# Performance work log

Measured on AMD Instinct MI355X. Metric: run time of the kernel, lower is better.

The kernel has to match this reference:

```python
import jax, jax.numpy as jnp
import numpy as np

D, VH, DFF, NL, VOCAB, NH, NKV, HD, R, SCALE = 4096, 1024, 14336, 2, 32000, 32, 8, 128, 8, 4.0
B, NIMG, T = 2, 257, 511
S = NIMG + T

def _rmsnorm(x, w, eps=1e-5):
    v = jnp.mean(jnp.square(x), axis=-1, keepdims=True)
    return x * jax.lax.rsqrt(v + eps) * w

def _lora(x, W, A, Bm):
    # base (dequantized NF4 equivalent) matmul + low-rank LoRA path, scaling = alpha/r
    base = jnp.einsum('...d,od->...o', x, W)
    low = jnp.einsum('...r,or->...o', jnp.einsum('...d,rd->...r', x, A), Bm)
    return base + low * SCALE

def _rope_tables(s):
    inv = 1.0 / (10000.0 ** (jnp.arange(0, HD, 2, dtype=jnp.float32) / HD))
    ang = jnp.arange(s, dtype=jnp.float32)[:, None] * inv[None, :]
    c, sn = jnp.cos(ang), jnp.sin(ang)
    return jnp.concatenate([c, c], -1), jnp.concatenate([sn, sn], -1)

def _apply_rope(x, cos, sin):
    rot = jnp.concatenate([-x[..., HD // 2:], x[..., :HD // 2]], -1)
    return x * cos + rot * sin

def _forward(image_embeds, proj_W, proj_b, embed, ln1, ln2, ln_f, Wq, Aq, Bq, Wk, Ak, Bk, Wv, Av, Bv, Wo, Ao, Bo, Wg, Ag, Bg, Wu, Au, Bu, Wd, Ad, Bd, input_ids, attention_mask):
    b = image_embeds.shape[0]
    img = jnp.einsum('bsv,dv->bsd', image_embeds, proj_W) + proj_b  # projector
    txt = embed[input_ids]                                          # token embedding lookup
    h = jnp.concatenate([img, txt], axis=1)                         # (B, S, D)
    s = h.shape[1]
    cos, sin = _rope_tables(s)
    allow = jnp.tril(jnp.ones((s, s), bool))[None, None] & (attention_mask[:, None, None, :] > 0)
    for i in range(NL):
        x = _rmsnorm(h, ln1[i])
        q = _lora(x, Wq[i], Aq[i], Bq[i]).reshape(b, s, NH, HD).transpose(0, 2, 1, 3)
        k = _lora(x, Wk[i], Ak[i], Bk[i]).reshape(b, s, NKV, HD).transpose(0, 2, 1, 3)
        v = _lora(x, Wv[i], Av[i], Bv[i]).reshape(b, s, NKV, HD).transpose(0, 2, 1, 3)
        q = _apply_rope(q, cos, sin)
        k = _apply_rope(k, cos, sin)
        k = jnp.repeat(k, NH // NKV, axis=1)  # GQA: expand kv heads
        v = jnp.repeat(v, NH // NKV, axis=1)
        scores = jnp.einsum('bhsd,bhtd->bhst', q, k) / jnp.sqrt(jnp.float32(HD))
        scores = jnp.where(allow, scores, jnp.float32(-1e30))
        attn = jnp.einsum('bhst,bhtd->bhsd', jax.nn.softmax(scores, axis=-1), v)
        attn = attn.transpose(0, 2, 1, 3).reshape(b, s, D)
        h = h + _lora(attn, Wo[i], Ao[i], Bo[i])
        x = _rmsnorm(h, ln2[i])
        h = h + _lora(jax.nn.silu(_lora(x, Wg[i], Ag[i], Bg[i])) * _lora(x, Wu[i], Au[i], Bu[i]), Wd[i], Ad[i], Bd[i])
    return _rmsnorm(h, ln_f)  # HF hidden_states[-1] is post final norm

def setup_inputs():
    key = jax.random.key(0)
    ks = iter(jax.random.split(key, 40))
    n = lambda shape, sc=0.02: jax.random.normal(next(ks), shape, jnp.float32) * sc
    return dict(
        image_embeds=jax.random.normal(next(ks), (B, NIMG, VH), jnp.float32),
        input_ids=jax.random.randint(next(ks), (B, T), 0, VOCAB),
        attention_mask=jnp.ones((B, S), jnp.int32),
        proj_W=n((D, VH)), proj_b=jnp.zeros((D,), jnp.float32),
        embed=n((VOCAB, D)),
        ln1=jnp.ones((NL, D), jnp.float32), ln2=jnp.ones((NL, D), jnp.float32), ln_f=jnp.ones((D,), jnp.float32),
        Wq=n((NL, D, D)), Aq=n((NL, R, D)), Bq=n((NL, D, R)),
        Wk=n((NL, NKV * HD, D)), Ak=n((NL, R, D)), Bk=n((NL, NKV * HD, R)),
        Wv=n((NL, NKV * HD, D)), Av=n((NL, R, D)), Bv=n((NL, NKV * HD, R)),
        Wo=n((NL, D, D)), Ao=n((NL, R, D)), Bo=n((NL, D, R)),
        Wg=n((NL, DFF, D)), Ag=n((NL, R, D)), Bg=n((NL, DFF, R)),
        Wu=n((NL, DFF, D)), Au=n((NL, R, D)), Bu=n((NL, DFF, R)),
        Wd=n((NL, D, DFF)), Ad=n((NL, R, DFF)), Bd=n((NL, D, R)),
    )

def reference(image_embeds, input_ids, attention_mask, proj_W, proj_b, embed, ln1, ln2, ln_f, Wq, Aq, Bq, Wk, Ak, Bk, Wv, Av, Bv, Wo, Ao, Bo, Wg, Ag, Bg, Wu, Au, Bu, Wd, Ad, Bd):
    return _forward(image_embeds, proj_W, proj_b, embed, ln1, ln2, ln_f, Wq, Aq, Bq, Wk, Ak, Bk, Wv, Av, Bv, Wo, Ao, Bo, Wg, Ag, Bg, Wu, Au, Bu, Wd, Ad, Bd, input_ids, attention_mask)
```

## Files before the change

kernel.cpp:

```cpp
#include <hip/hip_runtime.h>
#include <hip/hip_bf16.h>
#include <cstdint>
#include <cstddef>

typedef unsigned short u16;
typedef unsigned int u32;
typedef __attribute__((ext_vector_type(8))) short short8;
typedef __attribute__((ext_vector_type(4))) short short4v;
typedef __attribute__((ext_vector_type(4))) float f32x4;

__device__ __forceinline__ u16 f2bf(float f) {
  u32 u = __float_as_uint(f);
  u32 r = (u + 0x7FFFu + ((u >> 16) & 1u)) >> 16;
  return (u16)r;
}
__device__ __forceinline__ float bf2f(u16 u) {
  return __uint_as_float(((u32)u) << 16);
}
__device__ __forceinline__ short f2bf_hw(float f) {
  union { __hip_bfloat16 h; u16 u; } c;
  c.h = __float2bfloat16(f);
  return (short)c.u;
}

__device__ __forceinline__ void gload_lds16(const void* g, void* l) {
  __builtin_amdgcn_global_load_lds((const __attribute__((address_space(1))) void*)g,
                                   (__attribute__((address_space(3))) void*)l, 16, 0, 0);
}

__global__ __launch_bounds__(256) void convert_w_kernel(const float* __restrict__ src,
    u16* __restrict__ dst, long n8) {
  long stride = (long)gridDim.x * 256;
  for (long i = (long)blockIdx.x * 256 + threadIdx.x; i < n8; i += stride) {
    const float* p = src + i * 8;
    float4 v0 = *(const float4*)p;
    float4 v1 = *(const float4*)(p + 4);
    uint4 w;
    w.x = (u32)(u16)f2bf_hw(v0.x) | ((u32)(u16)f2bf_hw(v0.y) << 16);
    w.y = (u32)(u16)f2bf_hw(v0.z) | ((u32)(u16)f2bf_hw(v0.w) << 16);
    w.z = (u32)(u16)f2bf_hw(v1.x) | ((u32)(u16)f2bf_hw(v1.y) << 16);
    w.w = (u32)(u16)f2bf_hw(v1.z) | ((u32)(u16)f2bf_hw(v1.w) << 16);
    *(uint4*)(dst + i * 8) = w;
  }
}

struct ConvJob { const float* src; u16* dst; long n8; };
struct GemmArgs {
  const u16* A; int M; int K; int lda;
  const float* W0; const float* LB0; int toff0;
  const float* W1; const float* LB1; int toff1;
  const float* W2; const float* LB2; int toff2;
  const u16* Wb0; const u16* Wb1; const u16* Wb2;
  int ldw;
  int seg1; int seg2;
  const float* t;
  const float* bias;
  const float* resid;
  float* outf; int ostride;
  u16* outb0; u16* outb1;
  int rowremap;
  float* outp;
  int ny_main;
  ConvJob cj[3];
};

template<int WMODE>
__global__ __launch_bounds__(256) void gemm_kernel(GemmArgs a) {
  __shared__ u16 Asm[2][128 * 64];
  __shared__ u16 BsmW[2][WMODE ? 128 * 64 : 128 * 128];
  const int tid = threadIdx.x;

  const int nconv = (int)gridDim.y - a.ny_main;
  if ((int)blockIdx.y < nconv) {
    if (blockIdx.z != 0) return;
    const long cb = (long)blockIdx.y * gridDim.x + blockIdx.x;
    const long cstr = (long)nconv * gridDim.x * 256;
#pragma unroll
    for (int j = 0; j < 3; j++) {
      const float* src = a.cj[j].src;
      if (!src) break;
      u16* dst = a.cj[j].dst;
      const long n8 = a.cj[j].n8;
      for (long i = cb * 256 + tid; i < n8; i += cstr) {
        const float* p = src + i * 8;
        float4 v0 = *(const float4*)p;
        float4 v1 = *(const float4*)(p + 4);
        uint4 w;
        w.x = (u32)(u16)f2bf_hw(v0.x) | ((u32)(u16)f2bf_hw(v0.y) << 16);
        w.y = (u32)(u16)f2bf_hw(v0.z) | ((u32)(u16)f2bf_hw(v0.w) << 16);
        w.z = (u32)(u16)f2bf_hw(v1.x) | ((u32)(u16)f2bf_hw(v1.y) << 16);
        w.w = (u32)(u16)f2bf_hw(v1.z) | ((u32)(u16)f2bf_hw(v1.w) << 16);
        *(uint4*)(dst + i * 8) = w;
      }
    }
    return;
  }
  const int yid = (int)blockIdx.y - nconv;

  const int nwg = gridDim.x * a.ny_main;
  const int bid0 = yid * gridDim.x + blockIdx.x;
  const int q = nwg >> 3, r = nwg & 7;
  const int xcd = bid0 & 7, pos = bid0 >> 3;
  const int nb = (xcd < r ? xcd * (q + 1) : r * (q + 1) + (xcd - r) * q) + pos;
  const int m0 = (nb % gridDim.x) * 128;
  const int n0 = (nb / gridDim.x) * 128;

  const float* W = a.W0; const u16* Wb = a.Wb0;
  const float* LB = a.LB0; int toff = a.toff0; int nbase = 0;
  if (a.seg2 && n0 >= a.seg2)      { W = a.W2; Wb = a.Wb2; LB = a.LB2; toff = a.toff2; nbase = a.seg2; }
  else if (a.seg1 && n0 >= a.seg1) { W = a.W1; Wb = a.Wb1; LB = a.LB1; toff = a.toff1; nbase = a.seg1; }
  const int koff = blockIdx.z * a.K;
  const u16* Ab = a.A + koff;
  const float* Wt = W + (size_t)(n0 - nbase) * a.ldw + koff;
  const u16* Wbt = Wb + (size_t)(n0 - nbase) * a.ldw + koff;

  const int lane = tid & 63, wid = tid >> 6;
  const int wr = wid >> 1, wcn = wid & 1;
  const int lrow = lane & 15, g = lane >> 4;
  const int arow = lane >> 3;
  const int aslot = (lane & 7) ^ arow;
  const int brow4 = lane >> 4;

  f32x4 acc[4][4] = {};

  auto dma_A = [&](int k0, int buf) {
#pragma unroll
    for (int i = 0; i < 4; i++) {
      int c = wid * 4 + i;
      const u16* src = Ab + (size_t)(m0 + c * 8 + arow) * a.lda + k0 + (aslot << 3);
      gload_lds16(src, &Asm[buf][c * 512]);
    }
  };
  auto dma_B = [&](int k0, int buf) {
    if (WMODE) {
#pragma unroll
      for (int i = 0; i < 4; i++) {
        int c = wid * 4 + i;
        const u16* src = Wbt + (size_t)(c * 8 + arow) * a.ldw + k0 + (aslot << 3);
        gload_lds16(src, &BsmW[buf][c * 512]);
      }
    } else {
      float* Bf = (float*)&BsmW[buf][0];
#pragma unroll
      for (int j = 0; j < 8; j++) {
        int rrow = wid * 32 + j * 4 + brow4;
        int sslot = (lane & 15) ^ (rrow & 7);
        const float* src = Wt + (size_t)rrow * a.ldw + k0 + (sslot << 2);
        gload_lds16(src, &Bf[(wid * 32 + j * 4) * 64]);
      }
    }
  };

  const int nk = a.K >> 6;
  dma_A(0, 0); dma_B(0, 0);
  if (nk > 1) { dma_A(64, 1); dma_B(64, 1); }

  for (int kt = 0; kt < nk; kt++) {
    const int cur = kt & 1;
    if (kt + 1 < nk) {
      if (WMODE) asm volatile("s_waitcnt vmcnt(8)" ::: "memory");
      else       asm volatile("s_waitcnt vmcnt(12)" ::: "memory");
    } else {
      asm volatile("s_waitcnt vmcnt(0)" ::: "memory");
    }
    __builtin_amdgcn_sched_barrier(0);
    __builtin_amdgcn_s_barrier();
    __builtin_amdgcn_sched_barrier(0);

    short8 af[4][2], bq[4][2];
#pragma unroll
    for (int mi = 0; mi < 4; mi++) {
      int row = wr * 64 + mi * 16 + lrow;
#pragma unroll
      for (int x = 0; x < 2; x++) {
        int s = x * 4 + g;
        af[mi][x] = *(const short8*)&Asm[cur][row * 64 + ((s ^ (lrow & 7)) << 3)];
      }
    }
#pragma unroll
    for (int ni = 0; ni < 4; ni++) {
      int row = wcn * 64 + ni * 16 + lrow;
      if (WMODE) {
#pragma unroll
        for (int x = 0; x < 2; x++) {
          int s = x * 4 + g;
          bq[ni][x] = *(const short8*)&BsmW[cur][row * 64 + ((s ^ (lrow & 7)) << 3)];
        }
      } else {
        const float* bp = (const float*)&BsmW[cur][0] + row * 64;
        int m = row & 7;
#pragma unroll
        for (int x = 0; x < 2; x++) {
          int sg0 = x * 8 + g * 2;
          f32x4 lo = *(const f32x4*)(bp + ((sg0 ^ m) << 2));
          f32x4 hi = *(const f32x4*)(bp + (((sg0 + 1) ^ m) << 2));
          short8 sv;
          sv[0] = f2bf_hw(lo[0]); sv[1] = f2bf_hw(lo[1]);
          sv[2] = f2bf_hw(lo[2]); sv[3] = f2bf_hw(lo[3]);
          sv[4] = f2bf_hw(hi[0]); sv[5] = f2bf_hw(hi[1]);
          sv[6] = f2bf_hw(hi[2]); sv[7] = f2bf_hw(hi[3]);
          bq[ni][x] = sv;
        }
      }
    }

    asm volatile("s_waitcnt lgkmcnt(0)" ::: "memory");
    __builtin_amdgcn_sched_barrier(0);
    __builtin_amdgcn_s_barrier();
    __builtin_amdgcn_sched_barrier(0);
    if (kt + 2 < nk) {
      dma_A((kt + 2) << 6, cur);
      dma_B((kt + 2) << 6, cur);
    }
    __builtin_amdgcn_sched_barrier(0);
#pragma unroll
    for (int x = 0; x < 2; x++)
#pragma unroll
      for (int mi = 0; mi < 4; mi++)
#pragma unroll
        for (int ni = 0; ni < 4; ni++)
          acc[mi][ni] = __builtin_amdgcn_mfma_f32_16x16x32_bf16(af[mi][x], bq[ni][x], acc[mi][ni], 0, 0, 0);
  }

  if (a.outp) {
    float* op = a.outp + (size_t)blockIdx.z * (1536 * 4096);
#pragma unroll
    for (int mi = 0; mi < 4; mi++)
#pragma unroll
      for (int rr = 0; rr < 4; rr++) {
        int row = m0 + wr * 64 + mi * 16 + (g << 2) + rr;
#pragma unroll
        for (int ni = 0; ni < 4; ni++) {
          int n = n0 + wcn * 64 + ni * 16 + lrow;
          op[(size_t)row * a.ostride + n] = acc[mi][ni][rr];
        }
      }
    return;
  }
  const bool dolora = (a.t != nullptr);
  float lbv[4][8];
#pragma unroll
  for (int ni = 0; ni < 4; ni++) {
    if (dolora) {
      int cl = wcn * 64 + ni * 16 + lrow;
      const float* bp = LB + (size_t)(n0 - nbase + cl) * 8;
#pragma unroll
      for (int r2 = 0; r2 < 8; r2++) lbv[ni][r2] = bp[r2];
    }
  }
#pragma unroll
  for (int mi = 0; mi < 4; mi++) {
#pragma unroll
    for (int rr = 0; rr < 4; rr++) {
      int row = m0 + wr * 64 + mi * 16 + (g << 2) + rr;
      if (row >= a.M) continue;
      float tv[8];
      if (dolora) {
        const float* tp = a.t + row * 32 + toff;
#pragma unroll
        for (int r2 = 0; r2 < 8; r2++) tv[r2] = tp[r2];
      }
#pragma unroll
      for (int ni = 0; ni < 4; ni++) {
        int n = n0 + wcn * 64 + ni * 16 + lrow;
        float val = acc[mi][ni][rr];
        if (dolora) {
          float ds = 0.f;
#pragma unroll
          for (int r2 = 0; r2 < 8; r2++) ds += tv[r2] * lbv[ni][r2];
          val += 4.0f * ds;
        }
        if (a.bias)  val += a.bias[n];
        if (a.resid) val += a.resid[(size_t)row * 4096 + n];
        if (a.outf) {
          int orow = a.rowremap ? (row < 257 ? row : row + 511) : row;
          a.outf[(size_t)orow * a.ostride + n] = val;
        } else if (a.seg1 && n >= a.seg1) {
          a.outb1[(size_t)row * a.ostride + (n - a.seg1)] = f2bf(val);
        } else {
          a.outb0[(size_t)row * a.ostride + n] = f2bf(val);
        }
      }
    }
  }
}

__global__ __launch_bounds__(256) void combine_kernel(float* __restrict__ h,
    const float* __restrict__ p, const float* __restrict__ t,
    const float* __restrict__ LB) {
  const int row = blockIdx.x;
  float tv[8];
  const float* tp = t + row * 32;
#pragma unroll
  for (int r = 0; r < 8; r++) tv[r] = tp[r];
  const float* p1 = p + (size_t)1536 * 4096;
#pragma unroll
  for (int i = 0; i < 4; i++) {
    int base = threadIdx.x * 4 + i * 1024;
    size_t off = (size_t)row * 4096 + base;
    float4 hv = *(const float4*)(h + off);
    float4 a0 = *(const float4*)(p + off);
    float4 a1 = *(const float4*)(p1 + off);
    float o[4] = {hv.x + a0.x + a1.x, hv.y + a0.y + a1.y,
                  hv.z + a0.z + a1.z, hv.w + a0.w + a1.w};
#pragma unroll
    for (int j = 0; j < 4; j++) {
      const float* lb = LB + (size_t)(base + j) * 8;
      float ds = 0.f;
#pragma unroll
      for (int r = 0; r < 8; r++) ds += tv[r] * lb[r];
      o[j] += 4.0f * ds;
    }
    float4 ov; ov.x = o[0]; ov.y = o[1]; ov.z = o[2]; ov.w = o[3];
    *(float4*)(h + off) = ov;
  }
}

template<int NA>
__global__ __launch_bounds__(256) void lora_xa_kernel(const u16* __restrict__ X, int K,
    const float* A0, const float* A1, const float* A2, float* __restrict__ t) {
  const int m = blockIdx.x;
  const u16* xr = X + (size_t)m * K;
  float acc[NA * 8];
#pragma unroll
  for (int i = 0; i < NA * 8; i++) acc[i] = 0.f;
  const float* Ap[3] = {A0, A1, A2};
  for (int k = threadIdx.x * 8; k < K; k += 2048) {
    uint4 xv = *(const uint4*)(xr + k);
    float xf[8];
    xf[0] = bf2f((u16)(xv.x & 0xffff)); xf[1] = bf2f((u16)(xv.x >> 16));
    xf[2] = bf2f((u16)(xv.y & 0xffff)); xf[3] = bf2f((u16)(xv.y >> 16));
    xf[4] = bf2f((u16)(xv.z & 0xffff)); xf[5] = bf2f((u16)(xv.z >> 16));
    xf[6] = bf2f((u16)(xv.w & 0xffff)); xf[7] = bf2f((u16)(xv.w >> 16));
#pragma unroll
    for (int aa = 0; aa < NA; aa++) {
#pragma unroll
      for (int r = 0; r < 8; r++) {
        const float* ar = Ap[aa] + (size_t)r * K + k;
        float4 a0 = *(const float4*)ar;
        float4 a1 = *(const float4*)(ar + 4);
        acc[aa * 8 + r] += xf[0] * a0.x + xf[1] * a0.y + xf[2] * a0.z + xf[3] * a0.w
                         + xf[4] * a1.x + xf[5] * a1.y + xf[6] * a1.z + xf[7] * a1.w;
      }
    }
  }
  __shared__ float red[4][NA * 8];
#pragma unroll
  for (int i = 0; i < NA * 8; i++) {
    float v = acc[i];
#pragma unroll
    for (int o = 1; o < 64; o <<= 1) v += __shfl_xor(v, o);
    if ((threadIdx.x & 63) == 0) red[threadIdx.x >> 6][i] = v;
  }
  __syncthreads();
  if (threadIdx.x < NA * 8)
    t[m * 32 + threadIdx.x] = red[0][threadIdx.x] + red[1][threadIdx.x]
                            + red[2][threadIdx.x] + red[3][threadIdx.x];
}

__global__ __launch_bounds__(256) void rmsnorm_kernel(const float* __restrict__ h,
    const float* __restrict__ w, u16* outb, float* outf) {
  const int m = blockIdx.x;
  const float* row = h + (size_t)m * 4096;
  float4 v[4];
  float ss = 0.f;
#pragma unroll
  for (int i = 0; i < 4; i++) {
    v[i] = *(const float4*)(row + threadIdx.x * 4 + i * 1024);
    ss += v[i].x * v[i].x + v[i].y * v[i].y + v[i].z * v[i].z + v[i].w * v[i].w;
  }
#pragma unroll
  for (int o = 1; o < 64; o <<= 1) ss += __shfl_xor(ss, o);
  __shared__ float red[4];
  if ((threadIdx.x & 63) == 0) red[threadIdx.x >> 6] = ss;
  __syncthreads();
  ss = red[0] + red[1] + red[2] + red[3];
  float rs = rsqrtf(ss * (1.f / 4096.f) + 1e-5f);
#pragma unroll
  for (int i = 0; i < 4; i++) {
    int base = threadIdx.x * 4 + i * 1024;
    float4 wv = *(const float4*)(w + base);
    float o0 = v[i].x * rs * wv.x, o1 = v[i].y * rs * wv.y;
    float o2 = v[i].z * rs * wv.z, o3 = v[i].w * rs * wv.w;
    if (outb) {
      short4v sv; sv.x = (short)f2bf(o0); sv.y = (short)f2bf(o1);
      sv.z = (short)f2bf(o2); sv.w = (short)f2bf(o3);
      *(short4v*)(outb + (size_t)m * 4096 + base) = sv;
    } else {
      float4 ov; ov.x = o0; ov.y = o1; ov.z = o2; ov.w = o3;
      *(float4*)(outf + (size_t)m * 4096 + base) = ov;
    }
  }
}

__global__ void rope_tab_kernel(float2* __restrict__ tab) {
  int idx = blockIdx.x * 256 + threadIdx.x;
  int s = idx >> 6, i = idx & 63;
  float inv = __expf(-(float)i * (9.210340371976184f / 64.f));
  float ang = (float)s * inv;
  float sn, cs;
  sincosf(ang, &sn, &cs);
  float2 r; r.x = cs; r.y = sn;
  tab[idx] = r;
}

__global__ __launch_bounds__(256) void rope_apply_kernel(float* __restrict__ qkv,
    const float2* __restrict__ tab) {
  int m = blockIdx.x;
  int s = m % 768;
  float* rowp = qkv + (size_t)m * 6144;
  for (int idx = threadIdx.x; idx < 2560; idx += 256) {
    int head = idx >> 6, i = idx & 63;
    int col = (head < 32) ? head * 128 : 4096 + (head - 32) * 128;
    float2 cs = tab[s * 64 + i];
    float x0 = rowp[col + i], x1 = rowp[col + i + 64];
    rowp[col + i]      = x0 * cs.x - x1 * cs.y;
    rowp[col + i + 64] = x1 * cs.x + x0 * cs.y;
  }
}

__global__ __launch_bounds__(256) void attn_mfma_kernel(const float* __restrict__ qkv,
    const int* __restrict__ amask, u16* __restrict__ attn_bf) {
  __shared__ u16 Ks[4][32][40];
  __shared__ u16 Vt[128][40];
  __shared__ u16 Ps[4][16][40];
  const int b = blockIdx.z, hh = blockIdx.y, q0 = blockIdx.x * 64;
  const int kvh = hh >> 2;
  const int tid = threadIdx.x, lane = tid & 63, w = tid >> 6;
  const int lrow = lane & 15, g = lane >> 4;
  const float sc = 0.08838834764831845f;

  short8 qf[4];
  {
    const float* qp = qkv + ((size_t)(b * 768 + q0 + w * 16 + lrow)) * 6144 + hh * 128;
#pragma unroll
    for (int ks = 0; ks < 4; ks++) {
      float4 lo = *(const float4*)(qp + ks * 32 + g * 8);
      float4 hi = *(const float4*)(qp + ks * 32 + g * 8 + 4);
      short8 sv;
      sv[0] = f2bf_hw(lo.x * sc); sv[1] = f2bf_hw(lo.y * sc);
      sv[2] = f2bf_hw(lo.z * sc); sv[3] = f2bf_hw(lo.w * sc);
      sv[4] = f2bf_hw(hi.x * sc); sv[5] = f2bf_hw(hi.y * sc);
      sv[6] = f2bf_hw(hi.z * sc); sv[7] = f2bf_hw(hi.w * sc);
      qf[ks] = sv;
    }
  }

  f32x4 acco[8] = {};
  float mrun[4] = {-1e30f, -1e30f, -1e30f, -1e30f};
  float lrun[4] = {0.f, 0.f, 0.f, 0.f};
  const int ntile = (q0 >> 5) + 2;

  for (int kt = 0; kt < ntile; kt++) {
    const int k0 = kt * 32;
    __syncthreads();
#pragma unroll
    for (int i = 0; i < 4; i++) {
      int idx = i * 256 + tid;
      int r2 = idx >> 5, c4 = (idx & 31) << 2;
      const float* kp = qkv + ((size_t)(b * 768 + k0 + r2)) * 6144 + 4096 + kvh * 128 + c4;
      float4 kv = *(const float4*)kp;
      short4v ksv;
      ksv.x = f2bf_hw(kv.x); ksv.y = f2bf_hw(kv.y);
      ksv.z = f2bf_hw(kv.z); ksv.w = f2bf_hw(kv.w);
      *(short4v*)&Ks[c4 >> 5][r2][c4 & 31] = ksv;
      float4 vv = *(const float4*)(kp + 1024);
      Vt[c4 + 0][r2] = (u16)f2bf_hw(vv.x);
      Vt[c4 + 1][r2] = (u16)f2bf_hw(vv.y);
      Vt[c4 + 2][r2] = (u16)f2bf_hw(vv.z);
      Vt[c4 + 3][r2] = (u16)f2bf_hw(vv.w);
    }
    __syncthreads();

    f32x4 s0 = {}, s1 = {};
#pragma unroll
    for (int ks = 0; ks < 4; ks++) {
      short8 kb0 = *(const short8*)&Ks[ks][lrow][g * 8];
      short8 kb1 = *(const short8*)&Ks[ks][16 + lrow][g * 8];
      s0 = __builtin_amdgcn_mfma_f32_16x16x32_bf16(qf[ks], kb0, s0, 0, 0, 0);
      s1 = __builtin_amdgcn_mfma_f32_16x16x32_bf16(qf[ks], kb1, s1, 0, 0, 0);
    }
    const int key0 = k0 + lrow, key1 = k0 + 16 + lrow;
    const bool am0 = amask[b * 768 + key0] != 0;
    const bool am1 = amask[b * 768 + key1] != 0;
    float scl4[4];
#pragma unroll
    for (int rr = 0; rr < 4; rr++) {
      int qrow = q0 + w * 16 + g * 4 + rr;
      float v0 = (key0 <= qrow && am0) ? s0[rr] : -1e30f;
      float v1 = (key1 <= qrow && am1) ? s1[rr] : -1e30f;
      float m = fmaxf(v0, v1);
      m = fmaxf(m, __shfl_xor(m, 1));
      m = fmaxf(m, __shfl_xor(m, 2));
      m = fmaxf(m, __shfl_xor(m, 4));
      m = fmaxf(m, __shfl_xor(m, 8));
      float mnew = fmaxf(mrun[rr], m);
      float scl = __expf(mrun[rr] - mnew);
      float p0 = __expf(v0 - mnew);
      float p1 = __expf(v1 - mnew);
      float ls = p0 + p1;
      ls += __shfl_xor(ls, 1);
      ls += __shfl_xor(ls, 2);
      ls += __shfl_xor(ls, 4);
      ls += __shfl_xor(ls, 8);
      lrun[rr] = lrun[rr] * scl + ls;
      mrun[rr] = mnew;
      scl4[rr] = scl;
      Ps[w][g * 4 + rr][lrow]      = (u16)f2bf_hw(p0);
      Ps[w][g * 4 + rr][16 + lrow] = (u16)f2bf_hw(p1);
    }
#pragma unroll
    for (int nf = 0; nf < 8; nf++)
#pragma unroll
      for (int rr = 0; rr < 4; rr++) acco[nf][rr] *= scl4[rr];

    asm volatile("s_waitcnt lgkmcnt(0)" ::: "memory");
    __builtin_amdgcn_sched_barrier(0);
    short8 pa = *(const short8*)&Ps[w][lrow][g * 8];
#pragma unroll
    for (int nf = 0; nf < 8; nf++) {
      short8 vb = *(const short8*)&Vt[nf * 16 + lrow][g * 8];
      acco[nf] = __builtin_amdgcn_mfma_f32_16x16x32_bf16(pa, vb, acco[nf], 0, 0, 0);
    }
  }

#pragma unroll
  for (int rr = 0; rr < 4; rr++) {
    float inv = 1.f / lrun[rr];
    size_t orow = (size_t)(b * 768 + q0 + w * 16 + g * 4 + rr);
#pragma unroll
    for (int nf = 0; nf < 8; nf++)
      attn_bf[orow * 4096 + hh * 128 + nf * 16 + lrow] = f2bf(acco[nf][rr] * inv);
  }
}

__global__ void convert_img_kernel(const float* __restrict__ in, u16* __restrict__ out) {
  int idx = blockIdx.x * 256 + threadIdx.x;
  if (idx >= 81920) return;
  uint4 w = {0u, 0u, 0u, 0u};
  if (idx < 65792) {
    const float* p = in + (size_t)idx * 8;
    float4 v0 = *(const float4*)p;
    float4 v1 = *(const float4*)(p + 4);
    w.x = (u32)f2bf(v0.x) | ((u32)f2bf(v0.y) << 16);
    w.y = (u32)f2bf(v0.z) | ((u32)f2bf(v0.w) << 16);
    w.z = (u32)f2bf(v1.x) | ((u32)f2bf(v1.y) << 16);
    w.w = (u32)f2bf(v1.z) | ((u32)f2bf(v1.w) << 16);
  }
  *(uint4*)(out + (size_t)idx * 8) = w;
}

__global__ void embed_gather_kernel(const float* __restrict__ embed,
    const int* __restrict__ ids, float* __restrict__ h) {
  int row = blockIdx.x;
  int b = row / 511, tt = row % 511;
  int id = ids[b * 511 + tt];
  const float* src = embed + (size_t)id * 4096;
  float* dst = h + ((size_t)(b * 768 + 257 + tt)) * 4096;
  for (int i = threadIdx.x * 4; i < 4096; i += 1024)
    *(float4*)(dst + i) = *(const float4*)(src + i);
}

__global__ __launch_bounds__(256) void gu_combine_kernel(const u16* __restrict__ g,
    const u16* __restrict__ u, u16* __restrict__ x2) {
  size_t idx = (size_t)blockIdx.x * 256 + threadIdx.x;
  uint4 gv = *(const uint4*)(g + idx * 8);
  uint4 uv = *(const uint4*)(u + idx * 8);
  u32 gi[4] = {gv.x, gv.y, gv.z, gv.w};
  u32 ui[4] = {uv.x, uv.y, uv.z, uv.w};
  u32 oi[4];
#pragma unroll
  for (int i = 0; i < 4; i++) {
    float g0 = bf2f((u16)(gi[i] & 0xffff)), g1 = bf2f((u16)(gi[i] >> 16));
    float u0 = bf2f((u16)(ui[i] & 0xffff)), u1 = bf2f((u16)(ui[i] >> 16));
    float s0 = g0 / (1.f + __expf(-g0)) * u0;
    float s1 = g1 / (1.f + __expf(-g1)) * u1;
    oi[i] = (u32)f2bf(s0) | ((u32)f2bf(s1) << 16);
  }
  uint4 ov; ov.x = oi[0]; ov.y = oi[1]; ov.z = oi[2]; ov.w = oi[3];
  *(uint4*)(x2 + idx * 8) = ov;
}

extern "C" void kernel_launch(void* const* d_in, const int* in_sizes, int n_in,
                              void* d_out, int out_size, void* d_ws, size_t ws_size,
                              hipStream_t stream) {
  const float* image_embeds = (const float*)d_in[0];
  const int*   input_ids    = (const int*)d_in[1];
  const int*   amask        = (const int*)d_in[2];
  const float* proj_W = (const float*)d_in[3];
  const float* proj_b = (const float*)d_in[4];
  const float* embed  = (const float*)d_in[5];
  const float* ln1 = (const float*)d_in[6];
  const float* ln2 = (const float*)d_in[7];
  const float* ln_f = (const float*)d_in[8];
  const float* Wq = (const float*)d_in[9];
  const float* Aq = (const float*)d_in[10];
  const float* Bq = (const float*)d_in[11];
  const float* Wk = (const float*)d_in[12];
  const float* Ak = (const float*)d_in[13];
  const float* Bk = (const float*)d_in[14];
  const float* Wv = (const float*)d_in[15];
  const float* Av = (const float*)d_in[16];
  const float* Bv = (const float*)d_in[17];
  const float* Wo = (const float*)d_in[18];
  const float* Ao = (const float*)d_in[19];
  const float* Bo = (const float*)d_in[20];
  const float* Wg = (const float*)d_in[21];
  const float* Ag = (const float*)d_in[22];
  const float* Bg = (const float*)d_in[23];
  const float* Wu = (const float*)d_in[24];
  const float* Au = (const float*)d_in[25];
  const float* Bu = (const float*)d_in[26];
  const float* Wd = (const float*)d_in[27];
  const float* Ad = (const float*)d_in[28];
  const float* Bd = (const float*)d_in[29];
  (void)in_sizes; (void)n_in; (void)out_size;

  char* ws = (char*)d_ws;
  size_t off = 0;
  auto alloc = [&](size_t bytes) -> void* {
    void* p = ws + off; off += (bytes + 255) & ~(size_t)255; return p;
  };
  float* h       = (float*) alloc((size_t)1536 * 4096 * 4);
  u16*   xn      = (u16*)   alloc((size_t)1536 * 4096 * 2);
  float* qkv     = (float*) alloc((size_t)1536 * 6144 * 4);
  u16*   attn_bf = (u16*)   alloc((size_t)1536 * 4096 * 2);
  u16*   g_bf    = (u16*)   alloc((size_t)1536 * 14336 * 2);
  u16*   u_bf    = (u16*)   alloc((size_t)1536 * 14336 * 2);
  u16*   x2_bf   = (u16*)   alloc((size_t)1536 * 14336 * 2);
  float* t       = (float*) alloc((size_t)1536 * 32 * 4);
  float2* tab    = (float2*)alloc((size_t)768 * 64 * 8);
  u16*   img_bf  = (u16*)   alloc((size_t)640 * 1024 * 2);
  float* pc      = (float*) alloc((size_t)2 * 1536 * 4096 * 4);
  const size_t nQ = (size_t)2 * 4096 * 4096;
  const size_t nK = (size_t)2 * 1024 * 4096;
  const size_t nG = (size_t)2 * 14336 * 4096;
  const long nQl8 = 4096L * 4096 / 8, nKl8 = 1024L * 4096 / 8, nGl8 = 14336L * 4096 / 8;
  u16* wq_b = (u16*)alloc(nQ * 2);
  u16* wk_b = (u16*)alloc(nK * 2);
  u16* wv_b = (u16*)alloc(nK * 2);
  u16* wo_b = (u16*)alloc(nQ * 2);
  u16* wg_b = (u16*)alloc(nG * 2);
  u16* wu_b = (u16*)alloc(nG * 2);
  u16* wd_b = (u16*)alloc(nG * 2);
  const bool use_bf = (off <= ws_size);
  const int CONVY = 16;

  dim3 blk(256);
  if (use_bf) {
    convert_w_kernel<<<dim3(512), blk, 0, stream>>>(Wq, wq_b, nQl8);
    convert_w_kernel<<<dim3(256), blk, 0, stream>>>(Wk, wk_b, nKl8);
    convert_w_kernel<<<dim3(256), blk, 0, stream>>>(Wv, wv_b, nKl8);
  }
  auto launch_gemm = [&](const GemmArgs& a, dim3 grid) {
    if (a.Wb0) gemm_kernel<1><<<grid, blk, 0, stream>>>(a);
    else       gemm_kernel<0><<<grid, blk, 0, stream>>>(a);
  };

  convert_img_kernel<<<dim3(320), blk, 0, stream>>>(image_embeds, img_bf);
  rope_tab_kernel<<<dim3(192), blk, 0, stream>>>(tab);

  {
    GemmArgs a = {};
    a.A = img_bf; a.M = 514; a.K = 1024; a.lda = 1024; a.ldw = 1024;
    a.W0 = proj_W;
    a.bias = proj_b;
    a.outf = h; a.ostride = 4096; a.rowremap = 1;
    a.ny_main = 32;
    launch_gemm(a, dim3(5, 32));
  }
  embed_gather_kernel<<<dim3(1022), blk, 0, stream>>>(embed, input_ids, h);

  for (int l = 0; l < 2; l++) {
    const float* Wq_l = Wq + (size_t)l * 4096 * 4096;
    const float* Aq_l = Aq + (size_t)l * 8 * 4096;
    const float* Bq_l = Bq + (size_t)l * 4096 * 8;
    const float* Wk_l = Wk + (size_t)l * 1024 * 4096;
    const float* Ak_l = Ak + (size_t)l * 8 * 4096;
    const float* Bk_l = Bk + (size_t)l * 1024 * 8;
    const float* Wv_l = Wv + (size_t)l * 1024 * 4096;
    const float* Av_l = Av + (size_t)l * 8 * 4096;
    const float* Bv_l = Bv + (size_t)l * 1024 * 8;
    const float* Wo_l = Wo + (size_t)l * 4096 * 4096;
    const float* Ao_l = Ao + (size_t)l * 8 * 4096;
    const float* Bo_l = Bo + (size_t)l * 4096 * 8;
    const float* Wg_l = Wg + (size_t)l * 14336 * 4096;
    const float* Ag_l = Ag + (size_t)l * 8 * 4096;
    const float* Bg_l = Bg + (size_t)l * 14336 * 8;
    const float* Wu_l = Wu + (size_t)l * 14336 * 4096;
    const float* Au_l = Au + (size_t)l * 8 * 4096;
    const float* Bu_l = Bu + (size_t)l * 14336 * 8;
    const float* Wd_l = Wd + (size_t)l * 4096 * 14336;
    const float* Ad_l = Ad + (size_t)l * 8 * 14336;
    const float* Bd_l = Bd + (size_t)l * 4096 * 8;
    u16* wq_bl = wq_b + (size_t)l * 4096 * 4096;
    u16* wk_bl = wk_b + (size_t)l * 1024 * 4096;
    u16* wv_bl = wv_b + (size_t)l * 1024 * 4096;
    u16* wo_bl = wo_b + (size_t)l * 4096 * 4096;
    u16* wg_bl = wg_b + (size_t)l * 14336 * 4096;
    u16* wu_bl = wu_b + (size_t)l * 14336 * 4096;
    u16* wd_bl = wd_b + (size_t)l * 14336 * 4096;

    rmsnorm_kernel<<<dim3(1536), blk, 0, stream>>>(h, ln1 + l * 4096, xn, (float*)nullptr);
    lora_xa_kernel<3><<<dim3(1536), blk, 0, stream>>>(xn, 4096, Aq_l, Ak_l, Av_l, t);
    {
      GemmArgs a = {};
      a.A = xn; a.M = 1536; a.K = 4096; a.lda = 4096; a.ldw = 4096;
      a.W0 = Wq_l; a.LB0 = Bq_l; a.toff0 = 0;
      a.W1 = Wk_l; a.LB1 = Bk_l; a.toff1 = 8;
      a.W2 = Wv_l; a.LB2 = Bv_l; a.toff2 = 16;
      a.seg1 = 4096; a.seg2 = 5120;
      a.t = t; a.outf = qkv; a.ostride = 6144;
      a.ny_main = 48;
      dim3 grid(12, 48);
      if (use_bf) {
        a.Wb0 = wq_bl; a.Wb1 = wk_bl; a.Wb2 = wv_bl;
        a.cj[0] = {Wo_l, wo_bl, nQl8};
        a.cj[1] = {Wg_l, wg_bl, nGl8};
        grid = dim3(12, 48 + CONVY);
      }
      launch_gemm(a, grid);
    }
    rope_apply_kernel<<<dim3(1536), blk, 0, stream>>>(qkv, tab);
    attn_mfma_kernel<<<dim3(12, 32, 2), blk, 0, stream>>>(qkv, amask, attn_bf);
    lora_xa_kernel<1><<<dim3(1536), blk, 0, stream>>>(attn_bf, 4096, Ao_l,
        (const float*)nullptr, (const float*)nullptr, t);
    {
      GemmArgs a = {};
      a.A = attn_bf; a.M = 1536; a.K = 2048; a.lda = 4096; a.ldw = 4096;
      a.W0 = Wo_l;
      a.ostride = 4096; a.outp = pc;
      a.ny_main = 32;
      dim3 grid(12, 32, 2);
      if (use_bf) {
        a.Wb0 = wo_bl;
        a.cj[0] = {Wu_l, wu_bl, nGl8};
        grid = dim3(12, 32 + CONVY, 2);
      }
      launch_gemm(a, grid);
      combine_kernel<<<dim3(1536), blk, 0, stream>>>(h, pc, t, Bo_l);
    }
    rmsnorm_kernel<<<dim3(1536), blk, 0, stream>>>(h, ln2 + l * 4096, xn, (float*)nullptr);
    lora_xa_kernel<2><<<dim3(1536), blk, 0, stream>>>(xn, 4096, Ag_l, Au_l,
        (const float*)nullptr, t);
    {
      GemmArgs a = {};
      a.A = xn; a.M = 1536; a.K = 4096; a.lda = 4096; a.ldw = 4096;
      a.W0 = Wg_l; a.LB0 = Bg_l; a.toff0 = 0;
      a.W1 = Wu_l; a.LB1 = Bu_l; a.toff1 = 8;
      a.seg1 = 14336;
      a.t = t; a.outb0 = g_bf; a.outb1 = u_bf; a.ostride = 14336;
      a.ny_main = 224;
      dim3 grid(12, 224);
      if (use_bf) {
        a.Wb0 = wg_bl; a.Wb1 = wu_bl;
        a.cj[0] = {Wd_l, wd_bl, nGl8};
        grid = dim3(12, 224 + CONVY);
      }
      launch_gemm(a, grid);
    }
    gu_combine_kernel<<<dim3(10752), blk, 0, stream>>>(g_bf, u_bf, x2_bf);
    lora_xa_kernel<1><<<dim3(1536), blk, 0, stream>>>(x2_bf, 14336, Ad_l,
        (const float*)nullptr, (const float*)nullptr, t);
    {
      GemmArgs a = {};
      a.A = x2_bf; a.M = 1536; a.K = 7168; a.lda = 14336; a.ldw = 14336;
      a.W0 = Wd_l;
      a.ostride = 4096; a.outp = pc;
      a.ny_main = 32;
      dim3 grid(12, 32, 2);
      if (use_bf) {
        a.Wb0 = wd_bl;
        if (l == 0) {
          a.cj[0] = {Wq + (size_t)4096 * 4096, wq_b + (size_t)4096 * 4096, nQl8};
          a.cj[1] = {Wk + (size_t)1024 * 4096, wk_b + (size_t)1024 * 4096, nKl8};
          a.cj[2] = {Wv + (size_t)1024 * 4096, wv_b + (size_t)1024 * 4096, nKl8};
          grid = dim3(12, 32 + CONVY, 2);
        }
      }
      launch_gemm(a, grid);
      combine_kernel<<<dim3(1536), blk, 0, stream>>>(h, pc, t, Bd_l);
    }
  }
  rmsnorm_kernel<<<dim3(1536), blk, 0, stream>>>(h, ln_f, (u16*)nullptr, (float*)d_out);
}
```

Before: 3.043 ms.

## Fuse residual combine, RMSNorm and LoRA down-projection into single per-row kernels

Merges three per-row kernels into one: the residual combine (partial-sum add plus LoRA B up-projection), the following RMSNorm, and the LoRA A down-projection. The first layer's norm is also fused with its LoRA A projection, and the final norm is folded into the last combine. The goal is to cut several kernel launches and the extra full passes over the fp32 hidden state and the bf16 normalized activations. In exchange, each fused kernel holds more registers and performs more serial work per block.

```diff
diff --git a/kernel.cpp b/kernel.cpp
--- a/kernel.cpp
+++ b/kernel.cpp
@@ -285,19 +285,85 @@
   }
 }
 
-__global__ __launch_bounds__(256) void combine_kernel(float* __restrict__ h,
-    const float* __restrict__ p, const float* __restrict__ t,
-    const float* __restrict__ LB) {
-  const int row = blockIdx.x;
+
+template<int NA>
+__global__ __launch_bounds__(256) void fused_ln_lora_kernel(const float* __restrict__ h,
+    const float* __restrict__ w, u16* __restrict__ xn,
+    const float* A0, const float* A1, const float* A2, float* __restrict__ t) {
+  const int m = blockIdx.x, tid = threadIdx.x;
+  const float* row = h + (size_t)m * 4096;
+  float4 v[4];
+  float ss = 0.f;
+#pragma unroll
+  for (int i = 0; i < 4; i++) {
+    v[i] = *(const float4*)(row + tid * 4 + i * 1024);
+    ss += v[i].x * v[i].x + v[i].y * v[i].y + v[i].z * v[i].z + v[i].w * v[i].w;
+  }
+#pragma unroll
+  for (int o = 1; o < 64; o <<= 1) ss += __shfl_xor(ss, o);
+  __shared__ float red[4];
+  if ((tid & 63) == 0) red[tid >> 6] = ss;
+  __syncthreads();
+  ss = red[0] + red[1] + red[2] + red[3];
+  float rs = rsqrtf(ss * (1.f / 4096.f) + 1e-5f);
+  float xf[4][4];
+#pragma unroll
+  for (int i = 0; i < 4; i++) {
+    int base = tid * 4 + i * 1024;
+    float4 wv = *(const float4*)(w + base);
+    short4v sv;
+    sv.x = f2bf_hw(v[i].x * rs * wv.x); sv.y = f2bf_hw(v[i].y * rs * wv.y);
+    sv.z = f2bf_hw(v[i].z * rs * wv.z); sv.w = f2bf_hw(v[i].w * rs * wv.w);
+    *(short4v*)(xn + (size_t)m * 4096 + base) = sv;
+    xf[i][0] = bf2f((u16)sv.x); xf[i][1] = bf2f((u16)sv.y);
+    xf[i][2] = bf2f((u16)sv.z); xf[i][3] = bf2f((u16)sv.w);
+  }
+  const float* Ap[3] = {A0, A1, A2};
+  float part[NA * 8];
+#pragma unroll
+  for (int aa = 0; aa < NA; aa++)
+#pragma unroll
+    for (int r = 0; r < 8; r++) {
+      const float* ar = Ap[aa] + (size_t)r * 4096;
+      float acc = 0.f;
+#pragma unroll
+      for (int i = 0; i < 4; i++) {
+        float4 av = *(const float4*)(ar + tid * 4 + i * 1024);
+        acc += xf[i][0] * av.x + xf[i][1] * av.y + xf[i][2] * av.z + xf[i][3] * av.w;
+      }
+      part[aa * 8 + r] = acc;
+    }
+  __shared__ float red2[4][NA * 8];
+#pragma unroll
+  for (int i = 0; i < NA * 8; i++) {
+    float vv = part[i];
+#pragma unroll
+    for (int o = 1; o < 64; o <<= 1) vv += __shfl_xor(vv, o);
+    if ((tid & 63) == 0) red2[tid >> 6][i] = vv;
+  }
+  __syncthreads();
+  if (tid < NA * 8)
+    t[m * 32 + tid] = red2[0][tid] + red2[1][tid] + red2[2][tid] + red2[3][tid];
+}
+
+template<int NA>
+__global__ __launch_bounds__(256) void fused_combine_ln_kernel(float* __restrict__ h,
+    const float* __restrict__ p, const float* __restrict__ tL,
+    const float* __restrict__ LB, const float* __restrict__ w,
+    u16* __restrict__ xn, float* __restrict__ outf,
+    const float* A0, const float* A1, const float* A2, float* __restrict__ t) {
+  const int m = blockIdx.x, tid = threadIdx.x;
   float tv[8];
-  const float* tp = t + row * 32;
+  const float* tp = tL + m * 32;
 #pragma unroll
   for (int r = 0; r < 8; r++) tv[r] = tp[r];
   const float* p1 = p + (size_t)1536 * 4096;
+  float4 v[4];
+  float ss = 0.f;
 #pragma unroll
   for (int i = 0; i < 4; i++) {
-    int base = threadIdx.x * 4 + i * 1024;
-    size_t off = (size_t)row * 4096 + base;
+    int base = tid * 4 + i * 1024;
+    size_t off = (size_t)m * 4096 + base;
     float4 hv = *(const float4*)(h + off);
     float4 a0 = *(const float4*)(p + off);
     float4 a1 = *(const float4*)(p1 + off);
@@ -311,9 +377,70 @@
       for (int r = 0; r < 8; r++) ds += tv[r] * lb[r];
       o[j] += 4.0f * ds;
     }
-    float4 ov; ov.x = o[0]; ov.y = o[1]; ov.z = o[2]; ov.w = o[3];
-    *(float4*)(h + off) = ov;
-  }
+    v[i].x = o[0]; v[i].y = o[1]; v[i].z = o[2]; v[i].w = o[3];
+    if (NA > 0) *(float4*)(h + off) = v[i];
+    ss += o[0] * o[0] + o[1] * o[1] + o[2] * o[2] + o[3] * o[3];
+  }
+#pragma unroll
+  for (int o = 1; o < 64; o <<= 1) ss += __shfl_xor(ss, o);
+  __shared__ float red[4];
+  if ((tid & 63) == 0) red[tid >> 6] = ss;
+  __syncthreads();
+  ss = red[0] + red[1] + red[2] + red[3];
+  float rs = rsqrtf(ss * (1.f / 4096.f) + 1e-5f);
+
+  if (NA == 0) {
+#pragma unroll
+    for (int i = 0; i < 4; i++) {
+      int base = tid * 4 + i * 1024;
+      float4 wv = *(const float4*)(w + base);
+      float4 ov;
+      ov.x = v[i].x * rs * wv.x; ov.y = v[i].y * rs * wv.y;
+      ov.z = v[i].z * rs * wv.z; ov.w = v[i].w * rs * wv.w;
+      *(float4*)(outf + (size_t)m * 4096 + base) = ov;
+    }
+    return;
+  }
+
+  float xf[4][4];
+#pragma unroll
+  for (int i = 0; i < 4; i++) {
+    int base = tid * 4 + i * 1024;
+    float4 wv = *(const float4*)(w + base);
+    short4v sv;
+    sv.x = f2bf_hw(v[i].x * rs * wv.x); sv.y = f2bf_hw(v[i].y * rs * wv.y);
+    sv.z = f2bf_hw(v[i].z * rs * wv.z); sv.w = f2bf_hw(v[i].w * rs * wv.w);
+    *(short4v*)(xn + (size_t)m * 4096 + base) = sv;
+    xf[i][0] = bf2f((u16)sv.x); xf[i][1] = bf2f((u16)sv.y);
+    xf[i][2] = bf2f((u16)sv.z); xf[i][3] = bf2f((u16)sv.w);
+  }
+  const float* Ap[3] = {A0, A1, A2};
+  constexpr int NR = (NA > 0 ? NA : 1) * 8;
+  float part[NR];
+#pragma unroll
+  for (int aa = 0; aa < NA; aa++)
+#pragma unroll
+    for (int r = 0; r < 8; r++) {
+      const float* ar = Ap[aa] + (size_t)r * 4096;
+      float acc = 0.f;
+#pragma unroll
+      for (int i = 0; i < 4; i++) {
+        float4 av = *(const float4*)(ar + tid * 4 + i * 1024);
+        acc += xf[i][0] * av.x + xf[i][1] * av.y + xf[i][2] * av.z + xf[i][3] * av.w;
+      }
+      part[aa * 8 + r] = acc;
+    }
+  __shared__ float red2[4][NR];
+#pragma unroll
+  for (int i = 0; i < NA * 8; i++) {
+    float vv = part[i];
+#pragma unroll
+    for (int o = 1; o < 64; o <<= 1) vv += __shfl_xor(vv, o);
+    if ((tid & 63) == 0) red2[tid >> 6][i] = vv;
+  }
+  __syncthreads();
+  if (tid < NA * 8)
+    t[m * 32 + tid] = red2[0][tid] + red2[1][tid] + red2[2][tid] + red2[3][tid];
 }
 
 template<int NA>
@@ -671,25 +798,22 @@
   }
   embed_gather_kernel<<<dim3(1022), blk, 0, stream>>>(embed, input_ids, h);
 
+  fused_ln_lora_kernel<3><<<dim3(1536), blk, 0, stream>>>(h, ln1, xn, Aq, Ak, Av, t);
+
   for (int l = 0; l < 2; l++) {
     const float* Wq_l = Wq + (size_t)l * 4096 * 4096;
-    const float* Aq_l = Aq + (size_t)l * 8 * 4096;
     const float* Bq_l = Bq + (size_t)l * 4096 * 8;
     const float* Wk_l = Wk + (size_t)l * 1024 * 4096;
-    const float* Ak_l = Ak + (size_t)l * 8 * 4096;
     const float* Bk_l = Bk + (size_t)l * 1024 * 8;
     const float* Wv_l = Wv + (size_t)l * 1024 * 4096;
-    const float* Av_l = Av + (size_t)l * 8 * 4096;
     const float* Bv_l = Bv + (size_t)l * 1024 * 8;
     const float* Wo_l = Wo + (size_t)l * 4096 * 4096;
     const float* Ao_l = Ao + (size_t)l * 8 * 4096;
     const float* Bo_l = Bo + (size_t)l * 4096 * 8;
     const float* Wg_l = Wg + (size_t)l * 14336 * 4096;
     const float* Ag_l = Ag + (size_t)l * 8 * 4096;
-    const float* Bg_l = Bg + (size_t)l * 14336 * 8;
     const float* Wu_l = Wu + (size_t)l * 14336 * 4096;
     const float* Au_l = Au + (size_t)l * 8 * 4096;
-    const float* Bu_l = Bu + (size_t)l * 14336 * 8;
     const float* Wd_l = Wd + (size_t)l * 4096 * 14336;
     const float* Ad_l = Ad + (size_t)l * 8 * 14336;
     const float* Bd_l = Bd + (size_t)l * 4096 * 8;
@@ -701,8 +825,6 @@
     u16* wu_bl = wu_b + (size_t)l * 14336 * 4096;
     u16* wd_bl = wd_b + (size_t)l * 14336 * 4096;
 
-    rmsnorm_kernel<<<dim3(1536), blk, 0, stream>>>(h, ln1 + l * 4096, xn, (float*)nullptr);
-    lora_xa_kernel<3><<<dim3(1536), blk, 0, stream>>>(xn, 4096, Aq_l, Ak_l, Av_l, t);
     {
       GemmArgs a = {};
       a.A = xn; a.M = 1536; a.K = 4096; a.lda = 4096; a.ldw = 4096;
@@ -738,16 +860,14 @@
         grid = dim3(12, 32 + CONVY, 2);
       }
       launch_gemm(a, grid);
-      combine_kernel<<<dim3(1536), blk, 0, stream>>>(h, pc, t, Bo_l);
-    }
-    rmsnorm_kernel<<<dim3(1536), blk, 0, stream>>>(h, ln2 + l * 4096, xn, (float*)nullptr);
-    lora_xa_kernel<2><<<dim3(1536), blk, 0, stream>>>(xn, 4096, Ag_l, Au_l,
-        (const float*)nullptr, t);
+      fused_combine_ln_kernel<2><<<dim3(1536), blk, 0, stream>>>(h, pc, t, Bo_l,
+          ln2 + l * 4096, xn, (float*)nullptr, Ag_l, Au_l, (const float*)nullptr, t);
+    }
     {
       GemmArgs a = {};
       a.A = xn; a.M = 1536; a.K = 4096; a.lda = 4096; a.ldw = 4096;
-      a.W0 = Wg_l; a.LB0 = Bg_l; a.toff0 = 0;
-      a.W1 = Wu_l; a.LB1 = Bu_l; a.toff1 = 8;
+      a.W0 = Wg_l; a.LB0 = Bg + (size_t)l * 14336 * 8; a.toff0 = 0;
+      a.W1 = Wu_l; a.LB1 = Bu + (size_t)l * 14336 * 8; a.toff1 = 8;
       a.seg1 = 14336;
       a.t = t; a.outb0 = g_bf; a.outb1 = u_bf; a.ostride = 14336;
       a.ny_main = 224;
@@ -779,8 +899,16 @@
         }
       }
       launch_gemm(a, grid);
-      combine_kernel<<<dim3(1536), blk, 0, stream>>>(h, pc, t, Bd_l);
-    }
-  }
-  rmsnorm_kernel<<<dim3(1536), blk, 0, stream>>>(h, ln_f, (u16*)nullptr, (float*)d_out);
-}
+      if (l == 0) {
+        fused_combine_ln_kernel<3><<<dim3(1536), blk, 0, stream>>>(h, pc, t, Bd_l,
+            ln1 + 4096, xn, (float*)nullptr,
+            Aq + (size_t)8 * 4096, Ak + (size_t)8 * 4096, Av + (size_t)8 * 4096, t);
+      } else {
+        fused_combine_ln_kernel<0><<<dim3(1536), blk, 0, stream>>>(h, pc, t, Bd_l,
+            ln_f, (u16*)nullptr, (float*)d_out,
+            (const float*)nullptr, (const float*)nullptr, (const float*)nullptr,
+            (float*)nullptr);
+      }
+    }
+  }
+}
```

New measurement: 3.098 ms. No clear change (+1.8%).
